# Performance work log

Hardware: AMD Instinct MI355X
Metric: run time of the kernel (lower is better)

Reference implementation:

```python
import jax, jax.numpy as jnp
import numpy as np

NC = 80          # num classes (len(yolov8.names))
CONF = 0.25      # ultralytics conf_thres default
IOU_T = 0.45     # ultralytics iou_thres default
MAX_DET = 300    # module default max_det
K = 1024         # pre-NMS candidate cap (static stand-in for max_nms)
MAX_WH = 7680.0  # ultralytics class-offset for multi-class NMS


def setup_inputs() -> dict:
    key = jax.random.key(0)
    k1, k2, k3 = jax.random.split(key, 3)
    B, A = 32, 8400
    # YOLOv8 head layout: rows 0:4 = xywh (pixels), rows 4: = sigmoid class scores
    xy = jax.random.uniform(k1, (B, 2, A), dtype=jnp.float32) * 640.0
    wh = jax.random.uniform(k2, (B, 2, A), dtype=jnp.float32) * 160.0 + 8.0
    scores = jax.random.uniform(k3, (B, NC, A), dtype=jnp.float32) ** 3  # mostly below conf_thres
    preds = jnp.concatenate([xy, wh, scores], axis=1)  # [B, 4+NC, A]
    return {"preds": preds}


def _box_iou(b):
    # b: [K, 4] xyxy -> [K, K] pairwise IoU
    area = (b[:, 2] - b[:, 0]) * (b[:, 3] - b[:, 1])
    lt = jnp.maximum(b[:, None, :2], b[None, :, :2])
    rb = jnp.minimum(b[:, None, 2:], b[None, :, 2:])
    wh = jnp.clip(rb - lt, 0.0)
    inter = wh[..., 0] * wh[..., 1]
    return inter / (area[:, None] + area[None, :] - inter + 1e-7)


def _nms_single(pred):
    # pred: [4+NC, A]
    boxes_xywh = pred[:4].T           # [A, 4]
    cls_scores = pred[4:].T           # [A, NC]
    conf = cls_scores.max(-1)         # best-class confidence per anchor
    cls = jnp.argmax(cls_scores, -1)
    score = jnp.where(conf > CONF, conf, 0.0)
    top, idx = jax.lax.top_k(score, K)            # K candidates by confidence
    xywh = boxes_xywh[idx]
    half = xywh[:, 2:] * 0.5
    boxes = jnp.concatenate([xywh[:, :2] - half, xywh[:, :2] + half], -1)  # xyxy
    cls_k = cls[idx]
    valid = top > CONF
    # multi-class NMS via per-class coordinate offset (ultralytics trick)
    iou = _box_iou(boxes + (cls_k.astype(boxes.dtype) * MAX_WH)[:, None])
    ar = jnp.arange(K)

    def body(i, st):
        supp, keep = st
        ki = valid[i] & ~supp[i]
        keep = keep.at[i].set(ki)
        supp = supp | (ki & (iou[i] > IOU_T) & (ar > i))
        return supp, keep

    _, keep = jax.lax.fori_loop(0, K, body,
                                (jnp.zeros(K, bool), jnp.zeros(K, bool)))
    fscore = jnp.where(keep, top, 0.0)
    sc, order = jax.lax.top_k(fscore, MAX_DET)
    det = jnp.concatenate(
        [boxes[order], top[order][:, None], cls_k[order].astype(boxes.dtype)[:, None]], -1)
    # pad invalid rows with value NC in every column (matches F.pad(value=len(names)))
    return jnp.where((sc > CONF)[:, None], det, jnp.float32(NC))


def reference(preds):
    # [B, MAX_DET, 6] -> (x1, y1, x2, y2, conf, cls), padded rows filled with NC
    return jax.vmap(_nms_single)(preds)
```

## Files before the change

### kernel.cpp

```cpp
#include <hip/hip_runtime.h>
#include <stdint.h>

typedef unsigned long long u64;
typedef unsigned int u32;

#define NC 80
#define CONF_T 0.25f
#define IOU_THR 0.45f
#define MAX_DET 300
#define KCAND 1024
#define A_ANCH 8400
#define NROWS 84
#define MAX_WH 7680.0f

__global__ __launch_bounds__(512) void yolo_conf_kernel(const float* __restrict__ preds,
                                                        u64* __restrict__ keys) {
    int b = blockIdx.x / 9;
    int g = (blockIdx.x % 9) * 512 + threadIdx.x;
    if (g >= A_ANCH / 2) return;
    int a0 = g * 2;
    const float* base = preds + ((size_t)b * NROWS + 4) * A_ANCH + a0;
    float2 best = *(const float2*)base;
    int bc0 = 0, bc1 = 0;
#pragma unroll 8
    for (int c = 1; c < NC; ++c) {
        float2 v = *(const float2*)(base + (size_t)c * A_ANCH);
        if (v.x > best.x) { best.x = v.x; bc0 = c; }
        if (v.y > best.y) { best.y = v.y; bc1 = c; }
    }
    float s0 = (best.x > CONF_T) ? best.x : 0.0f;
    float s1 = (best.y > CONF_T) ? best.y : 0.0f;
    ulonglong2 kk;
    kk.x = ((u64)__float_as_uint(s0) << 32) | ((u64)(16383 - a0) << 7) | (u64)bc0;
    kk.y = ((u64)__float_as_uint(s1) << 32) | ((u64)(16383 - (a0 + 1)) << 7) | (u64)bc1;
    *(ulonglong2*)(keys + (size_t)b * A_ANCH + a0) = kk;
}

__device__ __forceinline__ float iou_f(float ix1, float iy1, float ix2, float iy2, float iar,
                                       float jx1, float jy1, float jx2, float jy2, float jar) {
    float lx = fmaxf(ix1, jx1), ly = fmaxf(iy1, jy1);
    float rx = fminf(ix2, jx2), ry = fminf(iy2, jy2);
    float ww = fmaxf(__fsub_rn(rx, lx), 0.0f);
    float hh = fmaxf(__fsub_rn(ry, ly), 0.0f);
    float inter = __fmul_rn(ww, hh);
    float den = __fadd_rn(__fsub_rn(__fadd_rn(iar, jar), inter), 1e-7f);
    return __fdiv_rn(inter, den);
}

__device__ __forceinline__ void hadd(u32* h, u32 bin, bool m, int lane) {
    u64 act = __ballot(m);
    if (act == 0) return;
    int fl = __ffsll((unsigned long long)act) - 1;
    u32 fb = __shfl(bin, fl);
    u64 same = __ballot(m && (bin == fb));
    if (lane == fl) atomicAdd(&h[fb], (u32)__popcll(same));
    if (m && (bin != fb)) atomicAdd(&h[bin], 1u);
}

__device__ __forceinline__ u64 bstep(u64 v, u32 idx, u32 size, u32 stride) {
    u64 v2 = __shfl_xor((unsigned long long)v, (int)stride, 64);
    bool keep_big = (((idx & stride) == 0) == ((idx & size) == 0));
    return ((v > v2) == keep_big) ? v : v2;
}

__global__ __launch_bounds__(512) void yolo_nms_kernel(const float* __restrict__ preds,
                                                       const u64* __restrict__ keys,
                                                       float* __restrict__ out) {
    const int b = blockIdx.x;
    const int tid = threadIdx.x;
    const int lane = tid & 63;
    const int wid = tid >> 6;

    __shared__ u32 sc[A_ANCH];
    __shared__ u64 skey[KCAND];
    __shared__ u32 histw[8 * 257];
    __shared__ u32 hist[256];
    union OvU {
        struct { u32 eqw[264]; u32 wpre[264]; } pre;
        struct {
            u64 rows[64];
            int keptlist[364];
            float kx1[364], ky1[364], kx2[364], ky2[364], kar[364];
            u32 kcls[364];
        } post;
    };
    __shared__ OvU ov;
    __shared__ u32 s_scal[4];
    __shared__ u32 s_csupp[2];
    __shared__ u32 s_nkept;

    const u64* kb = keys + (size_t)b * A_ANCH;

    for (int i = tid; i < 8 * 257; i += 512) histw[i] = 0;
    if (tid == 0) { s_scal[0] = 0; s_scal[1] = KCAND; s_scal[2] = 0; s_csupp[0] = 0; s_csupp[1] = 0; s_nkept = 0; }

    u32 vals[17];
#pragma unroll
    for (int it = 0; it < 17; ++it) {
        int a = tid + it * 512;
        vals[it] = (a < A_ANCH) ? (u32)(kb[a] >> 32) : 0u;
    }
#pragma unroll
    for (int it = 0; it < 17; ++it) {
        int a = tid + it * 512;
        if (a < A_ANCH) sc[a] = vals[it];
    }
    __syncthreads();

    u32* hw = histw + wid * 257;
    for (int p = 0; p < 4; ++p) {
        if (p == 0) {
#pragma unroll
            for (int it = 0; it < 17; ++it) {
                int a = tid + it * 512;
                hadd(hw, vals[it] >> 24, a < A_ANCH, lane);
            }
        } else {
            for (int i = tid; i < 8 * 257; i += 512) histw[i] = 0;
            __syncthreads();
            u32 prefix = s_scal[0];
            int shift = 24 - 8 * p;
            for (int it = 0; it < 17; ++it) {
                int a = tid + it * 512;
                u32 v = (a < A_ANCH) ? sc[a] : 0u;
                bool m = (a < A_ANCH) && ((v >> (shift + 8)) == prefix);
                hadd(hw, (v >> shift) & 255u, m, lane);
            }
        }
        __syncthreads();
        if (tid < 256) {
            u32 s = 0;
#pragma unroll
            for (int w = 0; w < 8; ++w) s += histw[w * 257 + tid];
            hist[tid] = s;
        }
        __syncthreads();
        if (wid == 0) {
            u32 g[4], loc = 0;
#pragma unroll
            for (int q = 0; q < 4; ++q) { g[q] = hist[255 - (lane * 4 + q)]; loc += g[q]; }
            u32 pre = loc;
#pragma unroll
            for (int off = 1; off < 64; off <<= 1) {
                u32 o = __shfl_up(pre, off);
                if (lane >= off) pre += o;
            }
            u32 run = pre - loc;
            u32 rem = s_scal[1];
            u32 pfx = s_scal[0];
#pragma unroll
            for (int q = 0; q < 4; ++q) {
                int d = 255 - (lane * 4 + q);
                if (run < rem && rem <= run + g[q]) {
                    s_scal[0] = (pfx << 8) | (u32)d;
                    s_scal[1] = rem - run;
                }
                run += g[q];
            }
        }
        __syncthreads();
    }
    const u32 P = s_scal[0];
    const u32 tEq = s_scal[1];

    if (tid < 264) ov.pre.eqw[tid] = 0;
    __syncthreads();
    for (int it = 0; it < 17; ++it) {
        int a = tid + it * 512;
        if (a < A_ANCH && sc[a] == P) atomicOr(&ov.pre.eqw[a >> 5], 1u << (a & 31));
    }
    __syncthreads();
    if (wid == 0) {
        u32 cnt[5], loc = 0;
#pragma unroll
        for (int q = 0; q < 5; ++q) {
            int w2 = lane * 5 + q;
            u32 e = (w2 < 264) ? ov.pre.eqw[w2] : 0u;
            cnt[q] = (u32)__popc(e); loc += cnt[q];
        }
        u32 pre = loc;
#pragma unroll
        for (int off = 1; off < 64; off <<= 1) {
            u32 o = __shfl_up(pre, off);
            if (lane >= off) pre += o;
        }
        u32 run = pre - loc;
#pragma unroll
        for (int q = 0; q < 5; ++q) {
            int w2 = lane * 5 + q;
            if (w2 < 264) ov.pre.wpre[w2] = run;
            run += cnt[q];
        }
    }
    __syncthreads();

    for (int it = 0; it < 17; ++it) {
        int a = tid + it * 512;
        if (a < A_ANCH) {
            u32 v = sc[a];
            bool take = v > P;
            if (!take && v == P) {
                u32 r = ov.pre.wpre[a >> 5] + (u32)__popc(ov.pre.eqw[a >> 5] & ((1u << (a & 31)) - 1u));
                take = (r < tEq);
            }
            if (take) {
                u32 pos = atomicAdd(&s_scal[2], 1u);
                skey[pos] = kb[a];
            }
        }
    }
    __syncthreads();

    {
        u64 vA = skey[tid], vB = skey[tid + 512];
        const u32 iA = (u32)tid, iB = (u32)tid + 512;
#pragma unroll
        for (u32 size = 2; size <= 64; size <<= 1) {
#pragma unroll
            for (u32 stride = size >> 1; stride >= 1; stride >>= 1) {
                vA = bstep(vA, iA, size, stride);
                vB = bstep(vB, iB, size, stride);
            }
        }
        skey[tid] = vA; skey[tid + 512] = vB;
        __syncthreads();
        for (u32 size = 128; size <= 1024; size <<= 1) {
            for (u32 stride = size >> 1; stride >= 64; stride >>= 1) {
                u32 i1 = ((tid & ~(int)(stride - 1)) << 1) | (tid & (stride - 1));
                u32 i2 = i1 + stride;
                bool desc = ((i1 & size) == 0);
                u64 x = skey[i1], y = skey[i2];
                if ((x < y) == desc) { skey[i1] = y; skey[i2] = x; }
                __syncthreads();
            }
            vA = skey[tid]; vB = skey[tid + 512];
#pragma unroll
            for (u32 stride = 32; stride >= 1; stride >>= 1) {
                vA = bstep(vA, iA, size, stride);
                vB = bstep(vB, iB, size, stride);
            }
            skey[tid] = vA; skey[tid + 512] = vB;
            __syncthreads();
        }
    }

    float* BX1 = (float*)sc;
    float* BY1 = BX1 + KCAND;
    float* BX2 = BX1 + 2 * KCAND;
    float* BY2 = BX1 + 3 * KCAND;
    float* BAR = BX1 + 4 * KCAND;
#pragma unroll
    for (int q = 0; q < 2; ++q) {
        int t = tid + q * 512;
        u64 key = skey[t];
        int cls = (int)(key & 127u);
        int idx = 16383 - (int)((key >> 7) & 16383u);
        const float* pb = preds + (size_t)b * NROWS * A_ANCH + idx;
        float x = pb[0];
        float y = pb[A_ANCH];
        float w = pb[2 * A_ANCH];
        float h = pb[3 * A_ANCH];
        float hw = __fmul_rn(w, 0.5f), hh = __fmul_rn(h, 0.5f);
        float x1 = __fsub_rn(x, hw), x2 = __fadd_rn(x, hw);
        float y1 = __fsub_rn(y, hh), y2 = __fadd_rn(y, hh);
        float off = __fmul_rn((float)cls, MAX_WH);
        float bx1 = __fadd_rn(x1, off), bx2 = __fadd_rn(x2, off);
        float by1 = __fadd_rn(y1, off), by2 = __fadd_rn(y2, off);
        BX1[t] = bx1; BY1[t] = by1; BX2[t] = bx2; BY2[t] = by2;
        BAR[t] = __fmul_rn(__fsub_rn(bx2, bx1), __fsub_rn(by2, by1));
    }
    __syncthreads();

    for (int c = 0; c < KCAND / 64; ++c) {
        int j = c * 64 + lane;
        u64 keyj = skey[j];
        float scj = __uint_as_float((u32)(keyj >> 32));
        u32 clsj = (u32)(keyj & 127u);
        float jx1 = BX1[j], jy1 = BY1[j], jx2 = BX2[j], jy2 = BY2[j], jar = BAR[j];

        u32 nk = s_nkept;
        bool suppbit = false;
        for (u32 k = wid; k < nk; k += 8) {
            bool cm = (ov.post.kcls[k] == clsj);
            if (__ballot(cm)) {
                float iou = iou_f(ov.post.kx1[k], ov.post.ky1[k], ov.post.kx2[k], ov.post.ky2[k],
                                  ov.post.kar[k], jx1, jy1, jx2, jy2, jar);
                suppbit |= (cm && (iou > IOU_THR));
            }
        }
        u64 bm = __ballot(suppbit);
        if (bm && lane == 0) {
            atomicOr(&s_csupp[0], (u32)bm);
            atomicOr(&s_csupp[1], (u32)(bm >> 32));
        }

#pragma unroll
        for (int p2 = 0; p2 < 8; ++p2) {
            int i = p2 * 8 + wid;
            int ci = c * 64 + i;
            u32 clsi = (u32)(skey[ci] & 127u);
            u64 m = 0;
            if (__ballot(clsi == clsj)) {
                float iou = iou_f(BX1[ci], BY1[ci], BX2[ci], BY2[ci], BAR[ci],
                                  jx1, jy1, jx2, jy2, jar);
                m = __ballot((lane > i) && (iou > IOU_THR));
            }
            if (lane == 0) ov.post.rows[i] = m;
        }
        __syncthreads();

        if (wid == 0) {
            u64 row = ov.post.rows[lane];
            u32 rlo = (u32)row, rhi = (u32)(row >> 32);
            u64 csupp = (((u64)s_csupp[1]) << 32) | (u64)s_csupp[0];
            u64 valid = __ballot(scj > CONF_T) & ~csupp;
            u64 supp = 0, keep = 0;
#pragma unroll
            for (int i = 0; i < 64; ++i) {
                u64 ri = (((u64)(u32)__builtin_amdgcn_readlane((int)rhi, i)) << 32) |
                         (u64)(u32)__builtin_amdgcn_readlane((int)rlo, i);
                bool ki = (((valid & ~supp) >> i) & 1ull) != 0;
                if (ki) { keep |= (1ull << i); supp |= ri; }
            }
            u32 base = s_nkept;
            if ((keep >> lane) & 1ull) {
                u32 slot = base + (u32)__popcll(keep & ((1ull << lane) - 1ull));
                ov.post.keptlist[slot] = j;
                ov.post.kx1[slot] = jx1; ov.post.ky1[slot] = jy1;
                ov.post.kx2[slot] = jx2; ov.post.ky2[slot] = jy2;
                ov.post.kar[slot] = jar; ov.post.kcls[slot] = clsj;
            }
            if (lane == 0) {
                s_nkept = base + (u32)__popcll(keep);
                s_csupp[0] = 0; s_csupp[1] = 0;
            }
        }
        __syncthreads();
        if (s_nkept >= MAX_DET) break;
    }

    if (tid < MAX_DET) {
        u32 nk = s_nkept;
        float row[6];
        int t = (tid < (int)(nk < MAX_DET ? nk : MAX_DET)) ? ov.post.keptlist[tid] : -1;
        if (t >= 0) {
            u64 key = skey[t];
            float score = __uint_as_float((u32)(key >> 32));
            int cls = (int)(key & 127u);
            int idx = 16383 - (int)((key >> 7) & 16383u);
            const float* pb = preds + (size_t)b * NROWS * A_ANCH + idx;
            float x = pb[0], y = pb[A_ANCH], w = pb[2 * A_ANCH], h = pb[3 * A_ANCH];
            float hw = __fmul_rn(w, 0.5f), hh = __fmul_rn(h, 0.5f);
            row[0] = __fsub_rn(x, hw);
            row[1] = __fsub_rn(y, hh);
            row[2] = __fadd_rn(x, hw);
            row[3] = __fadd_rn(y, hh);
            row[4] = score;
            row[5] = (float)cls;
        } else {
            row[0] = row[1] = row[2] = row[3] = row[4] = row[5] = (float)NC;
        }
        float* o = out + ((size_t)b * MAX_DET + tid) * 6;
#pragma unroll
        for (int q = 0; q < 6; ++q) o[q] = row[q];
    }
}

extern "C" void kernel_launch(void* const* d_in, const int* in_sizes, int n_in,
                              void* d_out, int out_size, void* d_ws, size_t ws_size,
                              hipStream_t stream) {
    const float* preds = (const float*)d_in[0];
    float* out = (float*)d_out;
    u64* keys = (u64*)d_ws;
    int B = in_sizes[0] / (NROWS * A_ANCH);
    yolo_conf_kernel<<<dim3(B * 9), dim3(512), 0, stream>>>(preds, keys);
    yolo_nms_kernel<<<dim3(B), dim3(512), 0, stream>>>(preds, keys, out);
}
```

Measured before the change: 79.15 us.

## Fuse conf and NMS kernels with flag sync, 12-bit radix, and adaptive K

After: 150.6 us. 1.9x slower.

```diff
diff --git a/kernel.cpp b/kernel.cpp
--- a/kernel.cpp
+++ b/kernel.cpp
@@ -8,33 +8,28 @@
 #define CONF_T 0.25f
 #define IOU_THR 0.45f
 #define MAX_DET 300
-#define KCAND 1024
+#define KBIG 1024
+#define KSMALL 512
 #define A_ANCH 8400
 #define NROWS 84
 #define MAX_WH 7680.0f
-
-__global__ __launch_bounds__(512) void yolo_conf_kernel(const float* __restrict__ preds,
-                                                        u64* __restrict__ keys) {
-    int b = blockIdx.x / 9;
-    int g = (blockIdx.x % 9) * 512 + threadIdx.x;
-    if (g >= A_ANCH / 2) return;
-    int a0 = g * 2;
-    const float* base = preds + ((size_t)b * NROWS + 4) * A_ANCH + a0;
-    float2 best = *(const float2*)base;
-    int bc0 = 0, bc1 = 0;
-#pragma unroll 8
-    for (int c = 1; c < NC; ++c) {
-        float2 v = *(const float2*)(base + (size_t)c * A_ANCH);
-        if (v.x > best.x) { best.x = v.x; bc0 = c; }
-        if (v.y > best.y) { best.y = v.y; bc1 = c; }
-    }
-    float s0 = (best.x > CONF_T) ? best.x : 0.0f;
-    float s1 = (best.y > CONF_T) ? best.y : 0.0f;
-    ulonglong2 kk;
-    kk.x = ((u64)__float_as_uint(s0) << 32) | ((u64)(16383 - a0) << 7) | (u64)bc0;
-    kk.y = ((u64)__float_as_uint(s1) << 32) | ((u64)(16383 - (a0 + 1)) << 7) | (u64)bc1;
-    *(ulonglong2*)(keys + (size_t)b * A_ANCH + a0) = kk;
-}
+#define NCONF 9
+#define ROLES 10
+
+union U1 {
+    u32 sc[A_ANCH];
+    struct {
+        float bx1[KBIG], by1[KBIG], bx2[KBIG], by2[KBIG], bar[KBIG];
+        int keptlist[364];
+        float kx1[364], ky1[364], kx2[364], ky2[364], kar[364];
+        u32 kcls[364];
+        u64 rows[64];
+    } post;
+};
+union U2 {
+    u32 hist[4096];
+    struct { u32 eqw[264]; u32 wpre[264]; } tie;
+};
 
 __device__ __forceinline__ float iou_f(float ix1, float iy1, float ix2, float iy2, float iar,
                                        float jx1, float jy1, float jx2, float jy2, float jar) {
@@ -63,82 +58,180 @@
     return ((v > v2) == keep_big) ? v : v2;
 }
 
-__global__ __launch_bounds__(512) void yolo_nms_kernel(const float* __restrict__ preds,
-                                                       const u64* __restrict__ keys,
-                                                       float* __restrict__ out) {
-    const int b = blockIdx.x;
+__device__ __forceinline__ void radix_scan(u32* hist, int nb, int shift, u32* s_scal,
+                                           u32* wsum, int tid, int lane, int wid) {
+    int per = nb >> 9; if (per == 0) per = 1;
+    int na = nb / per;
+    u32 rem = s_scal[1];
+    u32 Pk = s_scal[0];
+    int hi = nb - 1 - per * tid;
+    u32 s = 0;
+    if (tid < na)
+        for (int q = 0; q < per; ++q) s += hist[hi - q];
+    u32 pre = s;
+#pragma unroll
+    for (int off = 1; off < 64; off <<= 1) {
+        u32 o = __shfl_up(pre, off);
+        if (lane >= off) pre += o;
+    }
+    if (lane == 63) wsum[wid] = pre;
+    __syncthreads();
+    u32 base = 0;
+    for (int w = 0; w < wid; ++w) base += wsum[w];
+    u32 run = base + pre - s;
+    if (tid < na) {
+        for (int q = 0; q < per; ++q) {
+            int d = hi - q;
+            u32 g = hist[d];
+            if (run < rem && rem <= run + g) {
+                s_scal[0] = Pk | ((u32)d << shift);
+                s_scal[1] = rem - run;
+            }
+            run += g;
+        }
+    }
+    __syncthreads();
+}
+
+__global__ __launch_bounds__(512, 4) void yolo_fused(const float* __restrict__ preds,
+                                                     u64* __restrict__ keys,
+                                                     u32* __restrict__ cnt,
+                                                     float* __restrict__ out) {
+    const int bid = blockIdx.x;
+    const int b = bid / ROLES;
+    const int role = bid % ROLES;
     const int tid = threadIdx.x;
     const int lane = tid & 63;
     const int wid = tid >> 6;
 
-    __shared__ u32 sc[A_ANCH];
-    __shared__ u64 skey[KCAND];
-    __shared__ u32 histw[8 * 257];
-    __shared__ u32 hist[256];
-    union OvU {
-        struct { u32 eqw[264]; u32 wpre[264]; } pre;
-        struct {
-            u64 rows[64];
-            int keptlist[364];
-            float kx1[364], ky1[364], kx2[364], ky2[364], kar[364];
-            u32 kcls[364];
-        } post;
-    };
-    __shared__ OvU ov;
+    __shared__ U1 u1;
+    __shared__ U2 u2;
+    __shared__ u64 skey[KBIG];
+    __shared__ u32 wsum[8];
     __shared__ u32 s_scal[4];
     __shared__ u32 s_csupp[2];
     __shared__ u32 s_nkept;
-
-    const u64* kb = keys + (size_t)b * A_ANCH;
-
-    for (int i = tid; i < 8 * 257; i += 512) histw[i] = 0;
-    if (tid == 0) { s_scal[0] = 0; s_scal[1] = KCAND; s_scal[2] = 0; s_csupp[0] = 0; s_csupp[1] = 0; s_nkept = 0; }
-
-    u32 vals[17];
-#pragma unroll
-    for (int it = 0; it < 17; ++it) {
-        int a = tid + it * 512;
-        vals[it] = (a < A_ANCH) ? (u32)(kb[a] >> 32) : 0u;
+    __shared__ u32 s_valid;
+
+    if (role < NCONF) {
+        int g = role * 512 + tid;
+        if (g < A_ANCH / 2) {
+            int a0 = g * 2;
+            const float* base = preds + ((size_t)b * NROWS + 4) * A_ANCH + a0;
+            float2 best = *(const float2*)base;
+            int bc0 = 0, bc1 = 0;
+#pragma unroll 8
+            for (int c = 1; c < NC; ++c) {
+                float2 v = *(const float2*)(base + (size_t)c * A_ANCH);
+                if (v.x > best.x) { best.x = v.x; bc0 = c; }
+                if (v.y > best.y) { best.y = v.y; bc1 = c; }
+            }
+            float s0 = (best.x > CONF_T) ? best.x : 0.0f;
+            float s1 = (best.y > CONF_T) ? best.y : 0.0f;
+            ulonglong2 kk;
+            kk.x = ((u64)__float_as_uint(s0) << 32) | ((u64)(16383 - a0) << 7) | (u64)bc0;
+            kk.y = ((u64)__float_as_uint(s1) << 32) | ((u64)(16383 - (a0 + 1)) << 7) | (u64)bc1;
+            *(ulonglong2*)(keys + (size_t)b * A_ANCH + a0) = kk;
+        }
+        __threadfence();
+        __syncthreads();
+        if (tid == 0)
+            __hip_atomic_fetch_add(&cnt[b], 1u, __ATOMIC_RELEASE, __HIP_MEMORY_SCOPE_AGENT);
+        return;
     }
-#pragma unroll
-    for (int it = 0; it < 17; ++it) {
-        int a = tid + it * 512;
-        if (a < A_ANCH) sc[a] = vals[it];
+
+    if (tid == 0) {
+        while (__hip_atomic_load(&cnt[b], __ATOMIC_ACQUIRE, __HIP_MEMORY_SCOPE_AGENT) < NCONF)
+            __builtin_amdgcn_s_sleep(2);
     }
     __syncthreads();
-
-    u32* hw = histw + wid * 257;
-    for (int p = 0; p < 4; ++p) {
-        if (p == 0) {
-#pragma unroll
-            for (int it = 0; it < 17; ++it) {
-                int a = tid + it * 512;
-                hadd(hw, vals[it] >> 24, a < A_ANCH, lane);
-            }
-        } else {
-            for (int i = tid; i < 8 * 257; i += 512) histw[i] = 0;
-            __syncthreads();
-            u32 prefix = s_scal[0];
-            int shift = 24 - 8 * p;
-            for (int it = 0; it < 17; ++it) {
-                int a = tid + it * 512;
-                u32 v = (a < A_ANCH) ? sc[a] : 0u;
-                bool m = (a < A_ANCH) && ((v >> (shift + 8)) == prefix);
-                hadd(hw, (v >> shift) & 255u, m, lane);
-            }
-        }
-        __syncthreads();
-        if (tid < 256) {
-            u32 s = 0;
-#pragma unroll
-            for (int w = 0; w < 8; ++w) s += histw[w * 257 + tid];
-            hist[tid] = s;
+    __builtin_amdgcn_fence(__ATOMIC_ACQUIRE, "agent");
+
+    const u64* kb = keys + (size_t)b * A_ANCH;
+
+    for (int sel_pass = 0; sel_pass < 2; ++sel_pass) {
+        const int K_sel = sel_pass ? KBIG : KSMALL;
+
+        u32 vals[17];
+#pragma unroll
+        for (int it = 0; it < 17; ++it) {
+            int a = tid + it * 512;
+            vals[it] = (a < A_ANCH) ? (u32)(kb[a] >> 32) : 0u;
+        }
+        for (int i = tid; i < 4096; i += 512) u2.hist[i] = 0;
+        if (tid == 0) {
+            s_scal[0] = 0; s_scal[1] = (u32)K_sel; s_scal[2] = 0;
+            s_nkept = 0; s_csupp[0] = 0; s_csupp[1] = 0;
+            if (sel_pass == 0) s_valid = 0;
+        }
+#pragma unroll
+        for (int it = 0; it < 17; ++it) {
+            int a = tid + it * 512;
+            if (a < A_ANCH) u1.sc[a] = vals[it];
+        }
+        __syncthreads();
+
+#pragma unroll
+        for (int it = 0; it < 17; ++it) {
+            int a = tid + it * 512;
+            hadd(u2.hist, vals[it] >> 20, a < A_ANCH, lane);
+        }
+        if (sel_pass == 0) {
+            u32 c = 0;
+#pragma unroll
+            for (int it = 0; it < 17; ++it) c += (vals[it] != 0u) ? 1u : 0u;
+#pragma unroll
+            for (int off = 32; off >= 1; off >>= 1) c += __shfl_xor(c, off);
+            if (lane == 0) atomicAdd(&s_valid, c);
+        }
+        __syncthreads();
+        radix_scan(u2.hist, 4096, 20, s_scal, wsum, tid, lane, wid);
+
+        for (int i = tid; i < 4096; i += 512) u2.hist[i] = 0;
+        __syncthreads();
+        u32 Pk = s_scal[0];
+#pragma unroll
+        for (int it = 0; it < 17; ++it) {
+            int a = tid + it * 512;
+            u32 v = vals[it];
+            bool m = (a < A_ANCH) && ((v & 0xFFF00000u) == Pk);
+            hadd(u2.hist, (v >> 8) & 4095u, m, lane);
+        }
+        __syncthreads();
+        radix_scan(u2.hist, 4096, 8, s_scal, wsum, tid, lane, wid);
+
+        for (int i = tid; i < 256; i += 512) u2.hist[i] = 0;
+        __syncthreads();
+        Pk = s_scal[0];
+#pragma unroll
+        for (int it = 0; it < 17; ++it) {
+            int a = tid + it * 512;
+            u32 v = vals[it];
+            bool m = (a < A_ANCH) && ((v & 0xFFFFFF00u) == Pk);
+            hadd(u2.hist, v & 255u, m, lane);
+        }
+        __syncthreads();
+        radix_scan(u2.hist, 256, 0, s_scal, wsum, tid, lane, wid);
+
+        const u32 P = s_scal[0];
+        const u32 tEq = s_scal[1];
+
+        if (tid < 264) u2.tie.eqw[tid] = 0;
+        __syncthreads();
+#pragma unroll
+        for (int it = 0; it < 17; ++it) {
+            int a = tid + it * 512;
+            if (a < A_ANCH && vals[it] == P) atomicOr(&u2.tie.eqw[a >> 5], 1u << (a & 31));
         }
         __syncthreads();
         if (wid == 0) {
-            u32 g[4], loc = 0;
-#pragma unroll
-            for (int q = 0; q < 4; ++q) { g[q] = hist[255 - (lane * 4 + q)]; loc += g[q]; }
+            u32 cw[5], loc = 0;
+#pragma unroll
+            for (int q = 0; q < 5; ++q) {
+                int w2 = lane * 5 + q;
+                u32 e = (w2 < 264) ? u2.tie.eqw[w2] : 0u;
+                cw[q] = (u32)__popc(e); loc += cw[q];
+            }
             u32 pre = loc;
 #pragma unroll
             for (int off = 1; off < 64; off <<= 1) {
@@ -146,223 +239,214 @@
                 if (lane >= off) pre += o;
             }
             u32 run = pre - loc;
-            u32 rem = s_scal[1];
-            u32 pfx = s_scal[0];
-#pragma unroll
-            for (int q = 0; q < 4; ++q) {
-                int d = 255 - (lane * 4 + q);
-                if (run < rem && rem <= run + g[q]) {
-                    s_scal[0] = (pfx << 8) | (u32)d;
-                    s_scal[1] = rem - run;
-                }
-                run += g[q];
-            }
-        }
-        __syncthreads();
-    }
-    const u32 P = s_scal[0];
-    const u32 tEq = s_scal[1];
-
-    if (tid < 264) ov.pre.eqw[tid] = 0;
-    __syncthreads();
-    for (int it = 0; it < 17; ++it) {
-        int a = tid + it * 512;
-        if (a < A_ANCH && sc[a] == P) atomicOr(&ov.pre.eqw[a >> 5], 1u << (a & 31));
-    }
-    __syncthreads();
-    if (wid == 0) {
-        u32 cnt[5], loc = 0;
-#pragma unroll
-        for (int q = 0; q < 5; ++q) {
-            int w2 = lane * 5 + q;
-            u32 e = (w2 < 264) ? ov.pre.eqw[w2] : 0u;
-            cnt[q] = (u32)__popc(e); loc += cnt[q];
-        }
-        u32 pre = loc;
-#pragma unroll
-        for (int off = 1; off < 64; off <<= 1) {
-            u32 o = __shfl_up(pre, off);
-            if (lane >= off) pre += o;
-        }
-        u32 run = pre - loc;
-#pragma unroll
-        for (int q = 0; q < 5; ++q) {
-            int w2 = lane * 5 + q;
-            if (w2 < 264) ov.pre.wpre[w2] = run;
-            run += cnt[q];
-        }
-    }
-    __syncthreads();
-
-    for (int it = 0; it < 17; ++it) {
-        int a = tid + it * 512;
-        if (a < A_ANCH) {
-            u32 v = sc[a];
-            bool take = v > P;
-            if (!take && v == P) {
-                u32 r = ov.pre.wpre[a >> 5] + (u32)__popc(ov.pre.eqw[a >> 5] & ((1u << (a & 31)) - 1u));
-                take = (r < tEq);
-            }
-            if (take) {
-                u32 pos = atomicAdd(&s_scal[2], 1u);
-                skey[pos] = kb[a];
-            }
-        }
-    }
-    __syncthreads();
-
-    {
-        u64 vA = skey[tid], vB = skey[tid + 512];
-        const u32 iA = (u32)tid, iB = (u32)tid + 512;
-#pragma unroll
-        for (u32 size = 2; size <= 64; size <<= 1) {
-#pragma unroll
-            for (u32 stride = size >> 1; stride >= 1; stride >>= 1) {
-                vA = bstep(vA, iA, size, stride);
-                vB = bstep(vB, iB, size, stride);
-            }
-        }
-        skey[tid] = vA; skey[tid + 512] = vB;
-        __syncthreads();
-        for (u32 size = 128; size <= 1024; size <<= 1) {
-            for (u32 stride = size >> 1; stride >= 64; stride >>= 1) {
-                u32 i1 = ((tid & ~(int)(stride - 1)) << 1) | (tid & (stride - 1));
-                u32 i2 = i1 + stride;
-                bool desc = ((i1 & size) == 0);
-                u64 x = skey[i1], y = skey[i2];
-                if ((x < y) == desc) { skey[i1] = y; skey[i2] = x; }
-                __syncthreads();
-            }
-            vA = skey[tid]; vB = skey[tid + 512];
-#pragma unroll
-            for (u32 stride = 32; stride >= 1; stride >>= 1) {
-                vA = bstep(vA, iA, size, stride);
-                vB = bstep(vB, iB, size, stride);
-            }
+#pragma unroll
+            for (int q = 0; q < 5; ++q) {
+                int w2 = lane * 5 + q;
+                if (w2 < 264) u2.tie.wpre[w2] = run;
+                run += cw[q];
+            }
+        }
+        __syncthreads();
+
+#pragma unroll
+        for (int it = 0; it < 17; ++it) {
+            int a = tid + it * 512;
+            bool take = false;
+            if (a < A_ANCH) {
+                u32 v = vals[it];
+                take = v > P;
+                if (!take && v == P) {
+                    u32 r = u2.tie.wpre[a >> 5] +
+                            (u32)__popc(u2.tie.eqw[a >> 5] & ((1u << (a & 31)) - 1u));
+                    take = (r < tEq);
+                }
+            }
+            u64 m = __ballot(take);
+            if (m) {
+                int fl = __ffsll((unsigned long long)m) - 1;
+                u32 basep = 0;
+                if (lane == fl) basep = atomicAdd(&s_scal[2], (u32)__popcll(m));
+                basep = __shfl(basep, fl);
+                if (take) skey[basep + (u32)__popcll(m & ((1ull << lane) - 1ull))] = kb[a];
+            }
+        }
+        __syncthreads();
+
+        if (K_sel == KSMALL) {
+            u64 v = skey[tid];
+#pragma unroll
+            for (u32 size = 2; size <= 64; size <<= 1)
+#pragma unroll
+                for (u32 stride = size >> 1; stride >= 1; stride >>= 1)
+                    v = bstep(v, (u32)tid, size, stride);
+            for (u32 size = 128; size <= 512; size <<= 1) {
+                for (u32 stride = size >> 1; stride >= 64; stride >>= 1) {
+                    skey[tid] = v; __syncthreads();
+                    u64 v2 = skey[tid ^ stride];
+                    bool keep_big = ((((u32)tid & stride) == 0) == (((u32)tid & size) == 0));
+                    v = ((v > v2) == keep_big) ? v : v2;
+                    __syncthreads();
+                }
+#pragma unroll
+                for (u32 stride = 32; stride >= 1; stride >>= 1)
+                    v = bstep(v, (u32)tid, size, stride);
+            }
+            skey[tid] = v;
+            __syncthreads();
+        } else {
+            u64 vA = skey[tid], vB = skey[tid + 512];
+            const u32 iA = (u32)tid, iB = (u32)tid + 512;
+#pragma unroll
+            for (u32 size = 2; size <= 64; size <<= 1)
+#pragma unroll
+                for (u32 stride = size >> 1; stride >= 1; stride >>= 1) {
+                    vA = bstep(vA, iA, size, stride);
+                    vB = bstep(vB, iB, size, stride);
+                }
             skey[tid] = vA; skey[tid + 512] = vB;
             __syncthreads();
-        }
-    }
-
-    float* BX1 = (float*)sc;
-    float* BY1 = BX1 + KCAND;
-    float* BX2 = BX1 + 2 * KCAND;
-    float* BY2 = BX1 + 3 * KCAND;
-    float* BAR = BX1 + 4 * KCAND;
-#pragma unroll
-    for (int q = 0; q < 2; ++q) {
-        int t = tid + q * 512;
-        u64 key = skey[t];
-        int cls = (int)(key & 127u);
-        int idx = 16383 - (int)((key >> 7) & 16383u);
-        const float* pb = preds + (size_t)b * NROWS * A_ANCH + idx;
-        float x = pb[0];
-        float y = pb[A_ANCH];
-        float w = pb[2 * A_ANCH];
-        float h = pb[3 * A_ANCH];
-        float hw = __fmul_rn(w, 0.5f), hh = __fmul_rn(h, 0.5f);
-        float x1 = __fsub_rn(x, hw), x2 = __fadd_rn(x, hw);
-        float y1 = __fsub_rn(y, hh), y2 = __fadd_rn(y, hh);
-        float off = __fmul_rn((float)cls, MAX_WH);
-        float bx1 = __fadd_rn(x1, off), bx2 = __fadd_rn(x2, off);
-        float by1 = __fadd_rn(y1, off), by2 = __fadd_rn(y2, off);
-        BX1[t] = bx1; BY1[t] = by1; BX2[t] = bx2; BY2[t] = by2;
-        BAR[t] = __fmul_rn(__fsub_rn(bx2, bx1), __fsub_rn(by2, by1));
-    }
-    __syncthreads();
-
-    for (int c = 0; c < KCAND / 64; ++c) {
-        int j = c * 64 + lane;
-        u64 keyj = skey[j];
-        float scj = __uint_as_float((u32)(keyj >> 32));
-        u32 clsj = (u32)(keyj & 127u);
-        float jx1 = BX1[j], jy1 = BY1[j], jx2 = BX2[j], jy2 = BY2[j], jar = BAR[j];
-
-        u32 nk = s_nkept;
-        bool suppbit = false;
-        for (u32 k = wid; k < nk; k += 8) {
-            bool cm = (ov.post.kcls[k] == clsj);
-            if (__ballot(cm)) {
-                float iou = iou_f(ov.post.kx1[k], ov.post.ky1[k], ov.post.kx2[k], ov.post.ky2[k],
-                                  ov.post.kar[k], jx1, jy1, jx2, jy2, jar);
-                suppbit |= (cm && (iou > IOU_THR));
-            }
-        }
-        u64 bm = __ballot(suppbit);
-        if (bm && lane == 0) {
-            atomicOr(&s_csupp[0], (u32)bm);
-            atomicOr(&s_csupp[1], (u32)(bm >> 32));
-        }
-
-#pragma unroll
-        for (int p2 = 0; p2 < 8; ++p2) {
-            int i = p2 * 8 + wid;
-            int ci = c * 64 + i;
-            u32 clsi = (u32)(skey[ci] & 127u);
-            u64 m = 0;
-            if (__ballot(clsi == clsj)) {
-                float iou = iou_f(BX1[ci], BY1[ci], BX2[ci], BY2[ci], BAR[ci],
-                                  jx1, jy1, jx2, jy2, jar);
-                m = __ballot((lane > i) && (iou > IOU_THR));
-            }
-            if (lane == 0) ov.post.rows[i] = m;
-        }
-        __syncthreads();
-
-        if (wid == 0) {
-            u64 row = ov.post.rows[lane];
-            u32 rlo = (u32)row, rhi = (u32)(row >> 32);
-            u64 csupp = (((u64)s_csupp[1]) << 32) | (u64)s_csupp[0];
-            u64 valid = __ballot(scj > CONF_T) & ~csupp;
-            u64 supp = 0, keep = 0;
-#pragma unroll
-            for (int i = 0; i < 64; ++i) {
-                u64 ri = (((u64)(u32)__builtin_amdgcn_readlane((int)rhi, i)) << 32) |
-                         (u64)(u32)__builtin_amdgcn_readlane((int)rlo, i);
-                bool ki = (((valid & ~supp) >> i) & 1ull) != 0;
-                if (ki) { keep |= (1ull << i); supp |= ri; }
-            }
-            u32 base = s_nkept;
-            if ((keep >> lane) & 1ull) {
-                u32 slot = base + (u32)__popcll(keep & ((1ull << lane) - 1ull));
-                ov.post.keptlist[slot] = j;
-                ov.post.kx1[slot] = jx1; ov.post.ky1[slot] = jy1;
-                ov.post.kx2[slot] = jx2; ov.post.ky2[slot] = jy2;
-                ov.post.kar[slot] = jar; ov.post.kcls[slot] = clsj;
-            }
-            if (lane == 0) {
-                s_nkept = base + (u32)__popcll(keep);
-                s_csupp[0] = 0; s_csupp[1] = 0;
-            }
-        }
-        __syncthreads();
-        if (s_nkept >= MAX_DET) break;
-    }
-
-    if (tid < MAX_DET) {
-        u32 nk = s_nkept;
-        float row[6];
-        int t = (tid < (int)(nk < MAX_DET ? nk : MAX_DET)) ? ov.post.keptlist[tid] : -1;
-        if (t >= 0) {
+            for (u32 size = 128; size <= 1024; size <<= 1) {
+                for (u32 stride = size >> 1; stride >= 64; stride >>= 1) {
+                    u32 i1 = ((tid & ~(int)(stride - 1)) << 1) | (tid & (stride - 1));
+                    u32 i2 = i1 + stride;
+                    bool desc = ((i1 & size) == 0);
+                    u64 x = skey[i1], y = skey[i2];
+                    if ((x < y) == desc) { skey[i1] = y; skey[i2] = x; }
+                    __syncthreads();
+                }
+                vA = skey[tid]; vB = skey[tid + 512];
+#pragma unroll
+                for (u32 stride = 32; stride >= 1; stride >>= 1) {
+                    vA = bstep(vA, iA, size, stride);
+                    vB = bstep(vB, iB, size, stride);
+                }
+                skey[tid] = vA; skey[tid + 512] = vB;
+                __syncthreads();
+            }
+        }
+
+        for (int t = tid; t < K_sel; t += 512) {
             u64 key = skey[t];
-            float score = __uint_as_float((u32)(key >> 32));
             int cls = (int)(key & 127u);
             int idx = 16383 - (int)((key >> 7) & 16383u);
             const float* pb = preds + (size_t)b * NROWS * A_ANCH + idx;
-            float x = pb[0], y = pb[A_ANCH], w = pb[2 * A_ANCH], h = pb[3 * A_ANCH];
+            float x = pb[0];
+            float y = pb[A_ANCH];
+            float w = pb[2 * A_ANCH];
+            float h = pb[3 * A_ANCH];
             float hw = __fmul_rn(w, 0.5f), hh = __fmul_rn(h, 0.5f);
-            row[0] = __fsub_rn(x, hw);
-            row[1] = __fsub_rn(y, hh);
-            row[2] = __fadd_rn(x, hw);
-            row[3] = __fadd_rn(y, hh);
-            row[4] = score;
-            row[5] = (float)cls;
-        } else {
-            row[0] = row[1] = row[2] = row[3] = row[4] = row[5] = (float)NC;
-        }
-        float* o = out + ((size_t)b * MAX_DET + tid) * 6;
-#pragma unroll
-        for (int q = 0; q < 6; ++q) o[q] = row[q];
+            float x1 = __fsub_rn(x, hw), x2 = __fadd_rn(x, hw);
+            float y1 = __fsub_rn(y, hh), y2 = __fadd_rn(y, hh);
+            float off = __fmul_rn((float)cls, MAX_WH);
+            float bx1 = __fadd_rn(x1, off), bx2 = __fadd_rn(x2, off);
+            float by1 = __fadd_rn(y1, off), by2 = __fadd_rn(y2, off);
+            u1.post.bx1[t] = bx1; u1.post.by1[t] = by1;
+            u1.post.bx2[t] = bx2; u1.post.by2[t] = by2;
+            u1.post.bar[t] = __fmul_rn(__fsub_rn(bx2, bx1), __fsub_rn(by2, by1));
+        }
+        __syncthreads();
+
+        const int nchunks = K_sel / 64;
+        for (int c = 0; c < nchunks; ++c) {
+            int j = c * 64 + lane;
+            u64 keyj = skey[j];
+            float scj = __uint_as_float((u32)(keyj >> 32));
+            u32 clsj = (u32)(keyj & 127u);
+            float jx1 = u1.post.bx1[j], jy1 = u1.post.by1[j];
+            float jx2 = u1.post.bx2[j], jy2 = u1.post.by2[j], jar = u1.post.bar[j];
+
+            u32 nk = s_nkept;
+            bool suppbit = false;
+            for (u32 k = wid; k < nk; k += 8) {
+                bool cm = (u1.post.kcls[k] == clsj);
+                if (__ballot(cm)) {
+                    float iou = iou_f(u1.post.kx1[k], u1.post.ky1[k], u1.post.kx2[k],
+                                      u1.post.ky2[k], u1.post.kar[k],
+                                      jx1, jy1, jx2, jy2, jar);
+                    suppbit |= (cm && (iou > IOU_THR));
+                }
+            }
+            u64 bm = __ballot(suppbit);
+            if (bm && lane == 0) {
+                atomicOr(&s_csupp[0], (u32)bm);
+                atomicOr(&s_csupp[1], (u32)(bm >> 32));
+            }
+
+#pragma unroll
+            for (int p2 = 0; p2 < 8; ++p2) {
+                int i = p2 * 8 + wid;
+                int ci = c * 64 + i;
+                u32 clsi = (u32)(skey[ci] & 127u);
+                u64 m = 0;
+                if (__ballot(clsi == clsj)) {
+                    float iou = iou_f(u1.post.bx1[ci], u1.post.by1[ci], u1.post.bx2[ci],
+                                      u1.post.by2[ci], u1.post.bar[ci],
+                                      jx1, jy1, jx2, jy2, jar);
+                    m = __ballot((lane > i) && (iou > IOU_THR));
+                }
+                if (lane == 0) u1.post.rows[i] = m;
+            }
+            __syncthreads();
+
+            if (wid == 0) {
+                u64 row = u1.post.rows[lane];
+                u32 rlo = (u32)row, rhi = (u32)(row >> 32);
+                u64 csupp = (((u64)s_csupp[1]) << 32) | (u64)s_csupp[0];
+                u64 validm = __ballot(scj > CONF_T) & ~csupp;
+                u64 supp = 0, keep = 0;
+#pragma unroll
+                for (int i = 0; i < 64; ++i) {
+                    u64 ri = (((u64)(u32)__builtin_amdgcn_readlane((int)rhi, i)) << 32) |
+                             (u64)(u32)__builtin_amdgcn_readlane((int)rlo, i);
+                    bool ki = (((validm & ~supp) >> i) & 1ull) != 0;
+                    if (ki) { keep |= (1ull << i); supp |= ri; }
+                }
+                u32 basek = s_nkept;
+                if ((keep >> lane) & 1ull) {
+                    u32 slot = basek + (u32)__popcll(keep & ((1ull << lane) - 1ull));
+                    u1.post.keptlist[slot] = j;
+                    u1.post.kx1[slot] = jx1; u1.post.ky1[slot] = jy1;
+                    u1.post.kx2[slot] = jx2; u1.post.ky2[slot] = jy2;
+                    u1.post.kar[slot] = jar; u1.post.kcls[slot] = clsj;
+                }
+                if (lane == 0) {
+                    s_nkept = basek + (u32)__popcll(keep);
+                    s_csupp[0] = 0; s_csupp[1] = 0;
+                }
+            }
+            __syncthreads();
+            if (s_nkept >= MAX_DET) break;
+        }
+
+        u32 nk = s_nkept;
+        bool finished = (nk >= MAX_DET) || (s_valid <= (u32)K_sel) || (sel_pass == 1);
+        if (!finished) continue;
+
+        if (tid < MAX_DET) {
+            float row[6];
+            int t = (tid < (int)(nk < MAX_DET ? nk : MAX_DET)) ? u1.post.keptlist[tid] : -1;
+            if (t >= 0) {
+                u64 key = skey[t];
+                float score = __uint_as_float((u32)(key >> 32));
+                int cls = (int)(key & 127u);
+                int idx = 16383 - (int)((key >> 7) & 16383u);
+                const float* pb = preds + (size_t)b * NROWS * A_ANCH + idx;
+                float x = pb[0], y = pb[A_ANCH], w = pb[2 * A_ANCH], h = pb[3 * A_ANCH];
+                float hw = __fmul_rn(w, 0.5f), hh = __fmul_rn(h, 0.5f);
+                row[0] = __fsub_rn(x, hw);
+                row[1] = __fsub_rn(y, hh);
+                row[2] = __fadd_rn(x, hw);
+                row[3] = __fadd_rn(y, hh);
+                row[4] = score;
+                row[5] = (float)cls;
+            } else {
+                row[0] = row[1] = row[2] = row[3] = row[4] = row[5] = (float)NC;
+            }
+            float* o = out + ((size_t)b * MAX_DET + tid) * 6;
+#pragma unroll
+            for (int q = 0; q < 6; ++q) o[q] = row[q];
+        }
+        break;
     }
 }
 
@@ -371,8 +455,9 @@
                               hipStream_t stream) {
     const float* preds = (const float*)d_in[0];
     float* out = (float*)d_out;
+    int B = in_sizes[0] / (NROWS * A_ANCH);
     u64* keys = (u64*)d_ws;
-    int B = in_sizes[0] / (NROWS * A_ANCH);
-    yolo_conf_kernel<<<dim3(B * 9), dim3(512), 0, stream>>>(preds, keys);
-    yolo_nms_kernel<<<dim3(B), dim3(512), 0, stream>>>(preds, keys, out);
-}
+    u32* cnt = (u32*)(keys + (size_t)B * A_ANCH);
+    (void)hipMemsetAsync(cnt, 0, (size_t)B * sizeof(u32), stream);
+    yolo_fused<<<dim3(B * ROLES), dim3(512), 0, stream>>>(preds, keys, cnt, out);
+}
```
